# Performance work log

Measured on AMD Instinct MI355X. Metric: run time of the kernel, lower is better.

Reference implementation:

```python
import jax, jax.numpy as jnp
import numpy as np

N, DEG, D = 10000, 8, 128      # nodes, fixed out-degree, feature dim
E = N * DEG                    # graph edges = line-graph nodes
L = E * DEG                    # line-graph edges (fixed out-degree => exact)


def setup_inputs() -> dict:
    key = jax.random.key(0)
    kx, k1, k2 = jax.random.split(key, 3)
    rng = np.random.default_rng(0)

    # graph with fixed out-degree, no self-loops
    src = np.repeat(np.arange(N), DEG)                       # sorted by source
    dst = (src + 1 + rng.integers(0, N - 1, size=E)) % N
    edge_index = jnp.asarray(np.stack([src, dst]), dtype=jnp.int32)  # [2, E]

    # line graph: lg edge i -> j iff dst(i) == src(j)  (src(i)!=dst(i) holds for all i)
    # edges with source node v occupy indices v*DEG .. v*DEG+DEG-1
    lg_src = jnp.asarray(np.repeat(np.arange(E), DEG), dtype=jnp.int32)            # [L]
    lg_dst = jnp.asarray((dst[:, None] * DEG + np.arange(DEG)).reshape(-1),
                         dtype=jnp.int32)                                          # [L]

    x = jax.random.normal(kx, (N, D), jnp.float32)
    s = 1.0 / np.sqrt(D)
    ka, kb = jax.random.split(k1)
    W1 = jax.random.uniform(ka, (D, D), jnp.float32, -s, s)
    b1 = jnp.zeros((D,), jnp.float32)
    W2 = jax.random.uniform(kb, (D, D), jnp.float32, -s, s)
    b2 = jnp.zeros((D,), jnp.float32)
    return {"x": x, "edge_index": edge_index, "lg_src": lg_src, "lg_dst": lg_dst,
            "W1": W1, "b1": b1, "W2": W2, "b2": b2}


def reference(x, edge_index, lg_src, lg_dst, W1, b1, W2, b2):
    src, dst = edge_index[0], edge_index[1]
    # line-graph node features: mean of the two endpoint node features  [E, D]
    lgX = 0.5 * (x[src] + x[dst])
    # edge attr of lg edge (i->j) = feature of shared node = dst of source edge i  [L, D]
    edge_attr = x[dst[lg_src]]

    # 3 applications of the same GINEConv (eps=0, add aggregation)
    for _ in range(3):
        msg = jax.nn.relu(lgX[lg_src] + edge_attr)                      # [L, D]
        aggr = jax.ops.segment_sum(msg, lg_dst, num_segments=E)        # [E, D]
        h = lgX + aggr                                                  # (1+eps)*x_i + aggr, eps=0
        lgX = jax.nn.relu(h @ W1 + b1) @ W2 + b2

    # scatter_mean back to graph nodes over dst index, empty nodes -> 0 (matches pad)
    sums = jax.ops.segment_sum(lgX, dst, num_segments=N)               # [N, D]
    cnt = jax.ops.segment_sum(jnp.ones((E,), lgX.dtype), dst, num_segments=N)
    out = jax.nn.relu(sums / jnp.maximum(cnt, 1.0)[:, None])
    # dropout omitted (eval mode)
    return out
```

## Files before the change

kernel.cpp:

```cpp
#include <hip/hip_runtime.h>

#define NN 10000
#define EE 80000
#define DD 128
#define SLOTS 64

typedef short bf16x8 __attribute__((ext_vector_type(8)));
typedef float f32x4 __attribute__((ext_vector_type(4)));

__device__ __forceinline__ float b2f(uint u){ u <<= 16; return __builtin_bit_cast(float, u); }
__device__ __forceinline__ ushort f2b(float f){
  uint u = __builtin_bit_cast(uint, f);
  u += 0x7fffu + ((u >> 16) & 1u);
  return (ushort)(u >> 16);
}
__device__ __forceinline__ uint pack2(float a, float b){
  return (uint)f2b(a) | ((uint)f2b(b) << 16);
}

__global__ __launch_bounds__(256) void k_fill(const int* __restrict__ dst,
                                              int* __restrict__ cnt,
                                              int* __restrict__ inlist){
  int i = blockIdx.x * 256 + threadIdx.x;
  if (i < EE){
    int d = dst[i];
    int pos = atomicAdd(&cnt[d], 1);
    if (pos < SLOTS) inlist[d * SLOTS + pos] = i;
  }
}

__global__ __launch_bounds__(256) void k_wt(const float* __restrict__ W1, const float* __restrict__ W2,
                                            ushort* __restrict__ Wt1, ushort* __restrict__ Wt2){
  int idx = blockIdx.x * 256 + threadIdx.x;
  int which = idx >> 14;
  int r = idx & 16383;
  int k = r >> 7, n = r & 127;
  const float* W = which ? W2 : W1;
  ushort* Wt = which ? Wt2 : Wt1;
  Wt[n * DD + k] = f2b(W[r]);
}

__global__ __launch_bounds__(256) void k_init(const float* __restrict__ x, const int* __restrict__ dst,
                                              ushort* __restrict__ lgX){
  int tid = threadIdx.x;
  int i = blockIdx.x * 16 + (tid >> 4);
  int g = tid & 15;
  int s = i >> 3, d = dst[i];
  const float4* xs = (const float4*)(x + s * DD + g * 8);
  const float4* xd = (const float4*)(x + d * DD + g * 8);
  float4 s0 = xs[0], s1 = xs[1], d0 = xd[0], d1 = xd[1];
  uint4 o;
  o.x = pack2(0.5f * (s0.x + d0.x), 0.5f * (s0.y + d0.y));
  o.y = pack2(0.5f * (s0.z + d0.z), 0.5f * (s0.w + d0.w));
  o.z = pack2(0.5f * (s1.x + d1.x), 0.5f * (s1.y + d1.y));
  o.w = pack2(0.5f * (s1.z + d1.z), 0.5f * (s1.w + d1.w));
  *(uint4*)(lgX + i * DD + g * 8) = o;
}

__global__ __launch_bounds__(256) void k_aggr(const ushort* __restrict__ lgX, const float* __restrict__ x,
                                              const int* __restrict__ cnt, const int* __restrict__ inlist,
                                              float* __restrict__ A){
  int lane = threadIdx.x & 63;
  int v = blockIdx.x * 4 + (threadIdx.x >> 6);
  float2 xv = *(const float2*)(x + v * DD + lane * 2);
  int n = cnt[v]; if (n > SLOTS) n = SLOTS;
  float ax = 0.f, ay = 0.f;
  for (int t = 0; t < n; ++t){
    int e = inlist[v * SLOTS + t];
    uint u = *(const uint*)(lgX + e * DD + lane * 2);
    ax += fmaxf(b2f(u & 0xffffu) + xv.x, 0.f);
    ay += fmaxf(b2f(u >> 16)     + xv.y, 0.f);
  }
  float2 r; r.x = ax; r.y = ay;
  *(float2*)(A + v * DD + lane * 2) = r;
}

__global__ __launch_bounds__(256) void k_final(const ushort* __restrict__ lgX,
                                               const int* __restrict__ cnt, const int* __restrict__ inlist,
                                               float* __restrict__ out){
  int lane = threadIdx.x & 63;
  int v = blockIdx.x * 4 + (threadIdx.x >> 6);
  int n = cnt[v]; if (n > SLOTS) n = SLOTS;
  float ax = 0.f, ay = 0.f;
  for (int t = 0; t < n; ++t){
    int e = inlist[v * SLOTS + t];
    uint u = *(const uint*)(lgX + e * DD + lane * 2);
    ax += b2f(u & 0xffffu);
    ay += b2f(u >> 16);
  }
  float inv = 1.f / (float)(n > 0 ? n : 1);
  float2 r; r.x = fmaxf(ax * inv, 0.f); r.y = fmaxf(ay * inv, 0.f);
  *(float2*)(out + v * DD + lane * 2) = r;
}

__global__ __launch_bounds__(256, 2) void k_gemm(ushort* __restrict__ lgX, const float* __restrict__ A,
                                                 const ushort* __restrict__ Wt1, const ushort* __restrict__ Wt2,
                                                 const float* __restrict__ b1, const float* __restrict__ b2){
  __shared__ uint4 sm[4096];
  const int tid = threadIdx.x;
  const int lane = tid & 63;
  const int w = tid >> 6;
  const int rlo = lane & 15;
  const int khi = lane >> 4;
  const int row0 = blockIdx.x * 128;
  const bf16x8* smb = (const bf16x8*)sm;
  ushort* smh = (ushort*)sm;

  #pragma unroll
  for (int it = 0; it < 8; ++it){
    int gi = it * 256 + tid;
    int r = gi >> 4, g = gi & 15;
    sm[r * 16 + (g ^ (r & 7))] = *(const uint4*)(Wt1 + gi * 8);
  }
  #pragma unroll
  for (int p = 0; p < 8; ++p){
    int row = p * 16 + (tid >> 4);
    int g = tid & 15;
    int i = row0 + row;
    uint4 lx = *(const uint4*)(lgX + i * DD + g * 8);
    const float* Ap = A + (i >> 3) * DD + g * 8;
    float4 a0 = *(const float4*)Ap;
    float4 a1 = *(const float4*)(Ap + 4);
    uint uu[4] = {lx.x, lx.y, lx.z, lx.w};
    float av[8] = {a0.x, a0.y, a0.z, a0.w, a1.x, a1.y, a1.z, a1.w};
    float hv[8];
    #pragma unroll
    for (int j = 0; j < 4; ++j){
      hv[2*j]   = b2f(uu[j] & 0xffffu) + av[2*j];
      hv[2*j+1] = b2f(uu[j] >> 16)     + av[2*j+1];
    }
    uint4 o;
    o.x = pack2(hv[0], hv[1]); o.y = pack2(hv[2], hv[3]);
    o.z = pack2(hv[4], hv[5]); o.w = pack2(hv[6], hv[7]);
    sm[2048 + row * 16 + (g ^ (row & 7))] = o;
  }
  __syncthreads();

  f32x4 acc[2][8];
  #pragma unroll
  for (int m = 0; m < 2; ++m)
    #pragma unroll
    for (int nf = 0; nf < 8; ++nf) acc[m][nf] = (f32x4){0.f, 0.f, 0.f, 0.f};
  #pragma unroll
  for (int s = 0; s < 4; ++s){
    bf16x8 af[2];
    #pragma unroll
    for (int m = 0; m < 2; ++m){
      int row = 32 * w + 16 * m + rlo;
      int g = s * 4 + khi;
      af[m] = smb[2048 + row * 16 + (g ^ (row & 7))];
    }
    #pragma unroll
    for (int nf = 0; nf < 8; ++nf){
      int n = nf * 16 + rlo;
      int g = s * 4 + khi;
      bf16x8 bfr = smb[n * 16 + (g ^ (n & 7))];
      acc[0][nf] = __builtin_amdgcn_mfma_f32_16x16x32_bf16(af[0], bfr, acc[0][nf], 0, 0, 0);
      acc[1][nf] = __builtin_amdgcn_mfma_f32_16x16x32_bf16(af[1], bfr, acc[1][nf], 0, 0, 0);
    }
  }
  #pragma unroll
  for (int nf = 0; nf < 8; ++nf){
    float bb = b1[nf * 16 + rlo];
    #pragma unroll
    for (int m = 0; m < 2; ++m){
      #pragma unroll
      for (int q = 0; q < 4; ++q){
        float v = fmaxf(acc[m][nf][q] + bb, 0.f);
        int row = 32 * w + 16 * m + khi * 4 + q;
        int col = nf * 16 + rlo;
        smh[(2048 + row * 16 + ((col >> 3) ^ (row & 7))) * 8 + (col & 7)] = f2b(v);
      }
    }
  }
  __syncthreads();
  #pragma unroll
  for (int it = 0; it < 8; ++it){
    int gi = it * 256 + tid;
    int r = gi >> 4, g = gi & 15;
    sm[r * 16 + (g ^ (r & 7))] = *(const uint4*)(Wt2 + gi * 8);
  }
  __syncthreads();

  f32x4 acc2[2][8];
  #pragma unroll
  for (int m = 0; m < 2; ++m)
    #pragma unroll
    for (int nf = 0; nf < 8; ++nf) acc2[m][nf] = (f32x4){0.f, 0.f, 0.f, 0.f};
  #pragma unroll
  for (int s = 0; s < 4; ++s){
    bf16x8 af[2];
    #pragma unroll
    for (int m = 0; m < 2; ++m){
      int row = 32 * w + 16 * m + rlo;
      int g = s * 4 + khi;
      af[m] = smb[2048 + row * 16 + (g ^ (row & 7))];
    }
    #pragma unroll
    for (int nf = 0; nf < 8; ++nf){
      int n = nf * 16 + rlo;
      int g = s * 4 + khi;
      bf16x8 bfr = smb[n * 16 + (g ^ (n & 7))];
      acc2[0][nf] = __builtin_amdgcn_mfma_f32_16x16x32_bf16(af[0], bfr, acc2[0][nf], 0, 0, 0);
      acc2[1][nf] = __builtin_amdgcn_mfma_f32_16x16x32_bf16(af[1], bfr, acc2[1][nf], 0, 0, 0);
    }
  }
  #pragma unroll
  for (int nf = 0; nf < 8; ++nf){
    float bb = b2[nf * 16 + rlo];
    #pragma unroll
    for (int m = 0; m < 2; ++m){
      #pragma unroll
      for (int q = 0; q < 4; ++q){
        float v = acc2[m][nf][q] + bb;
        int row = 32 * w + 16 * m + khi * 4 + q;
        int col = nf * 16 + rlo;
        smh[(2048 + row * 16 + ((col >> 3) ^ (row & 7))) * 8 + (col & 7)] = f2b(v);
      }
    }
  }
  #pragma unroll
  for (int it = 0; it < 8; ++it){
    int u = it * 64 + lane;
    int row = 32 * w + (u >> 4);
    int g = u & 15;
    uint4 val = sm[2048 + row * 16 + (g ^ (row & 7))];
    *(uint4*)(lgX + (row0 + row) * DD + g * 8) = val;
  }
}

extern "C" void kernel_launch(void* const* d_in, const int* in_sizes, int n_in,
                              void* d_out, int out_size, void* d_ws, size_t ws_size,
                              hipStream_t stream){
  (void)in_sizes; (void)n_in; (void)out_size; (void)ws_size;
  const float* x  = (const float*)d_in[0];
  const int*   ei = (const int*)d_in[1];
  const int*   dst = ei + EE;
  const float* W1 = (const float*)d_in[4];
  const float* b1 = (const float*)d_in[5];
  const float* W2 = (const float*)d_in[6];
  const float* b2 = (const float*)d_in[7];
  float* out = (float*)d_out;

  char* ws = (char*)d_ws;
  ushort* lgX = (ushort*)ws;
  float*  A   = (float*)(ws + 20480000);
  ushort* Wt1 = (ushort*)(ws + 25600000);
  ushort* Wt2 = (ushort*)(ws + 25632768);
  int*    cnt = (int*)(ws + 25665536);
  int*    inl = (int*)(ws + 25705536);

  hipMemsetAsync(cnt, 0, NN * sizeof(int), stream);
  k_fill<<<(EE + 255) / 256, 256, 0, stream>>>(dst, cnt, inl);
  k_wt<<<128, 256, 0, stream>>>(W1, W2, Wt1, Wt2);
  k_init<<<EE / 16, 256, 0, stream>>>(x, dst, lgX);
  for (int it = 0; it < 3; ++it){
    k_aggr<<<NN / 4, 256, 0, stream>>>(lgX, x, cnt, inl, A);
    k_gemm<<<EE / 128, 256, 0, stream>>>(lgX, A, Wt1, Wt2, b1, b2);
  }
  k_final<<<NN / 4, 256, 0, stream>>>(lgX, cnt, inl, out);
}
```

Baseline: 212.5 us.

## Fuse setup kernels and restructure GEMM to keep H fragments in registers

```diff
diff --git a/kernel.cpp b/kernel.cpp
--- a/kernel.cpp
+++ b/kernel.cpp
@@ -18,43 +18,40 @@
   return (uint)f2b(a) | ((uint)f2b(b) << 16);
 }
 
-__global__ __launch_bounds__(256) void k_fill(const int* __restrict__ dst,
-                                              int* __restrict__ cnt,
-                                              int* __restrict__ inlist){
-  int i = blockIdx.x * 256 + threadIdx.x;
-  if (i < EE){
-    int d = dst[i];
-    int pos = atomicAdd(&cnt[d], 1);
-    if (pos < SLOTS) inlist[d * SLOTS + pos] = i;
-  }
-}
-
-__global__ __launch_bounds__(256) void k_wt(const float* __restrict__ W1, const float* __restrict__ W2,
-                                            ushort* __restrict__ Wt1, ushort* __restrict__ Wt2){
-  int idx = blockIdx.x * 256 + threadIdx.x;
-  int which = idx >> 14;
-  int r = idx & 16383;
-  int k = r >> 7, n = r & 127;
-  const float* W = which ? W2 : W1;
-  ushort* Wt = which ? Wt2 : Wt1;
-  Wt[n * DD + k] = f2b(W[r]);
-}
-
-__global__ __launch_bounds__(256) void k_init(const float* __restrict__ x, const int* __restrict__ dst,
-                                              ushort* __restrict__ lgX){
+__global__ __launch_bounds__(256) void k_pre(const float* __restrict__ x, const int* __restrict__ dst,
+                                             const float* __restrict__ W1, const float* __restrict__ W2,
+                                             ushort* __restrict__ lgX, ushort* __restrict__ Wt,
+                                             int* __restrict__ cnt, int* __restrict__ inlist){
+  int b = blockIdx.x;
   int tid = threadIdx.x;
-  int i = blockIdx.x * 16 + (tid >> 4);
-  int g = tid & 15;
-  int s = i >> 3, d = dst[i];
-  const float4* xs = (const float4*)(x + s * DD + g * 8);
-  const float4* xd = (const float4*)(x + d * DD + g * 8);
-  float4 s0 = xs[0], s1 = xs[1], d0 = xd[0], d1 = xd[1];
-  uint4 o;
-  o.x = pack2(0.5f * (s0.x + d0.x), 0.5f * (s0.y + d0.y));
-  o.y = pack2(0.5f * (s0.z + d0.z), 0.5f * (s0.w + d0.w));
-  o.z = pack2(0.5f * (s1.x + d1.x), 0.5f * (s1.y + d1.y));
-  o.w = pack2(0.5f * (s1.z + d1.z), 0.5f * (s1.w + d1.w));
-  *(uint4*)(lgX + i * DD + g * 8) = o;
+  if (b < 5000){
+    int i = b * 16 + (tid >> 4);
+    int g = tid & 15;
+    int s = i >> 3, d = dst[i];
+    const float4* xs = (const float4*)(x + s * DD + g * 8);
+    const float4* xd = (const float4*)(x + d * DD + g * 8);
+    float4 s0 = xs[0], s1 = xs[1], d0 = xd[0], d1 = xd[1];
+    uint4 o;
+    o.x = pack2(0.5f * (s0.x + d0.x), 0.5f * (s0.y + d0.y));
+    o.y = pack2(0.5f * (s0.z + d0.z), 0.5f * (s0.w + d0.w));
+    o.z = pack2(0.5f * (s1.x + d1.x), 0.5f * (s1.y + d1.y));
+    o.w = pack2(0.5f * (s1.z + d1.z), 0.5f * (s1.w + d1.w));
+    *(uint4*)(lgX + i * DD + g * 8) = o;
+  } else if (b < 5128){
+    int idx = (b - 5000) * 256 + tid;
+    int which = idx >> 14;
+    int r = idx & 16383;
+    int k = r >> 7, n = r & 127;
+    const float* W = which ? W2 : W1;
+    Wt[which * 16384 + n * DD + k] = f2b(W[r]);
+  } else {
+    int i = (b - 5128) * 256 + tid;
+    if (i < EE){
+      int d = dst[i];
+      int pos = atomicAdd(&cnt[d], 1);
+      if (pos < SLOTS) inlist[d * SLOTS + pos] = i;
+    }
+  }
 }
 
 __global__ __launch_bounds__(256) void k_aggr(const ushort* __restrict__ lgX, const float* __restrict__ x,
@@ -93,139 +90,137 @@
   *(float2*)(out + v * DD + lane * 2) = r;
 }
 
-__global__ __launch_bounds__(256, 2) void k_gemm(ushort* __restrict__ lgX, const float* __restrict__ A,
-                                                 const ushort* __restrict__ Wt1, const ushort* __restrict__ Wt2,
-                                                 const float* __restrict__ b1, const float* __restrict__ b2){
-  __shared__ uint4 sm[4096];
+__global__ __launch_bounds__(256) void k_gemm(ushort* __restrict__ lgX, const float* __restrict__ A,
+                                              const ushort* __restrict__ Wt,
+                                              const float* __restrict__ b1, const float* __restrict__ b2){
+  __shared__ uint4 smW[2048];
+  __shared__ uint4 smT[2048];
   const int tid = threadIdx.x;
   const int lane = tid & 63;
   const int w = tid >> 6;
   const int rlo = lane & 15;
   const int khi = lane >> 4;
   const int row0 = blockIdx.x * 128;
-  const bf16x8* smb = (const bf16x8*)sm;
-  ushort* smh = (ushort*)sm;
+  const bf16x8* smWb = (const bf16x8*)smW;
+  const bf16x8* smTb = (const bf16x8*)smT;
+  uint* smTu = (uint*)smT;
 
   #pragma unroll
   for (int it = 0; it < 8; ++it){
     int gi = it * 256 + tid;
     int r = gi >> 4, g = gi & 15;
-    sm[r * 16 + (g ^ (r & 7))] = *(const uint4*)(Wt1 + gi * 8);
-  }
-  #pragma unroll
-  for (int p = 0; p < 8; ++p){
-    int row = p * 16 + (tid >> 4);
-    int g = tid & 15;
-    int i = row0 + row;
-    uint4 lx = *(const uint4*)(lgX + i * DD + g * 8);
-    const float* Ap = A + (i >> 3) * DD + g * 8;
-    float4 a0 = *(const float4*)Ap;
-    float4 a1 = *(const float4*)(Ap + 4);
-    uint uu[4] = {lx.x, lx.y, lx.z, lx.w};
-    float av[8] = {a0.x, a0.y, a0.z, a0.w, a1.x, a1.y, a1.z, a1.w};
-    float hv[8];
-    #pragma unroll
-    for (int j = 0; j < 4; ++j){
-      hv[2*j]   = b2f(uu[j] & 0xffffu) + av[2*j];
-      hv[2*j+1] = b2f(uu[j] >> 16)     + av[2*j+1];
-    }
-    uint4 o;
-    o.x = pack2(hv[0], hv[1]); o.y = pack2(hv[2], hv[3]);
-    o.z = pack2(hv[4], hv[5]); o.w = pack2(hv[6], hv[7]);
-    sm[2048 + row * 16 + (g ^ (row & 7))] = o;
+    smW[r * 16 + (g ^ (r & 7))] = *(const uint4*)(Wt + gi * 8);
+  }
+
+  bf16x8 hfrag[2][4];
+  #pragma unroll
+  for (int mb = 0; mb < 2; ++mb){
+    int row = row0 + (2 * w + mb) * 16 + rlo;
+    const ushort* lp = lgX + row * DD;
+    const float*  ap = A + (row >> 3) * DD;
+    #pragma unroll
+    for (int s = 0; s < 4; ++s){
+      int k0 = s * 32 + khi * 8;
+      uint4 lx = *(const uint4*)(lp + k0);
+      float4 a0 = *(const float4*)(ap + k0);
+      float4 a1 = *(const float4*)(ap + k0 + 4);
+      uint uu[4] = {lx.x, lx.y, lx.z, lx.w};
+      float av[8] = {a0.x, a0.y, a0.z, a0.w, a1.x, a1.y, a1.z, a1.w};
+      uint4 o;
+      o.x = pack2(b2f(uu[0] & 0xffffu) + av[0], b2f(uu[0] >> 16) + av[1]);
+      o.y = pack2(b2f(uu[1] & 0xffffu) + av[2], b2f(uu[1] >> 16) + av[3]);
+      o.z = pack2(b2f(uu[2] & 0xffffu) + av[4], b2f(uu[2] >> 16) + av[5]);
+      o.w = pack2(b2f(uu[3] & 0xffffu) + av[6], b2f(uu[3] >> 16) + av[7]);
+      hfrag[mb][s] = __builtin_bit_cast(bf16x8, o);
+    }
   }
   __syncthreads();
 
-  f32x4 acc[2][8];
-  #pragma unroll
-  for (int m = 0; m < 2; ++m)
-    #pragma unroll
-    for (int nf = 0; nf < 8; ++nf) acc[m][nf] = (f32x4){0.f, 0.f, 0.f, 0.f};
+  f32x4 acc1[2][8];
+  #pragma unroll
+  for (int mb = 0; mb < 2; ++mb)
+    #pragma unroll
+    for (int nf = 0; nf < 8; ++nf) acc1[mb][nf] = (f32x4){0.f, 0.f, 0.f, 0.f};
   #pragma unroll
   for (int s = 0; s < 4; ++s){
-    bf16x8 af[2];
-    #pragma unroll
-    for (int m = 0; m < 2; ++m){
-      int row = 32 * w + 16 * m + rlo;
+    #pragma unroll
+    for (int nf = 0; nf < 8; ++nf){
+      int r = nf * 16 + rlo;
       int g = s * 4 + khi;
-      af[m] = smb[2048 + row * 16 + (g ^ (row & 7))];
-    }
-    #pragma unroll
-    for (int nf = 0; nf < 8; ++nf){
-      int n = nf * 16 + rlo;
+      bf16x8 wf = smWb[r * 16 + (g ^ (r & 7))];
+      acc1[0][nf] = __builtin_amdgcn_mfma_f32_16x16x32_bf16(wf, hfrag[0][s], acc1[0][nf], 0, 0, 0);
+      acc1[1][nf] = __builtin_amdgcn_mfma_f32_16x16x32_bf16(wf, hfrag[1][s], acc1[1][nf], 0, 0, 0);
+    }
+  }
+
+  #pragma unroll
+  for (int mb = 0; mb < 2; ++mb){
+    int row = (2 * w + mb) * 16 + rlo;
+    int rsw = row & 7;
+    #pragma unroll
+    for (int nf = 0; nf < 8; ++nf){
+      float4 bb = *(const float4*)(b1 + nf * 16 + khi * 4);
+      float t0 = fmaxf(acc1[mb][nf][0] + bb.x, 0.f);
+      float t1 = fmaxf(acc1[mb][nf][1] + bb.y, 0.f);
+      float t2 = fmaxf(acc1[mb][nf][2] + bb.z, 0.f);
+      float t3 = fmaxf(acc1[mb][nf][3] + bb.w, 0.f);
+      int u0 = nf * 8 + khi * 2;
+      int g0 = u0 >> 2;
+      int base = row * 64 + ((g0 ^ rsw) << 2) + (u0 & 3);
+      smTu[base]     = pack2(t0, t1);
+      smTu[base + 1] = pack2(t2, t3);
+    }
+  }
+
+  f32x4 acc2[2][8];
+  #pragma unroll
+  for (int mb = 0; mb < 2; ++mb)
+    #pragma unroll
+    for (int nf = 0; nf < 8; ++nf) acc2[mb][nf] = (f32x4){0.f, 0.f, 0.f, 0.f};
+  #pragma unroll
+  for (int s = 0; s < 4; ++s){
+    bf16x8 tf[2];
+    #pragma unroll
+    for (int mb = 0; mb < 2; ++mb){
+      int row = (2 * w + mb) * 16 + rlo;
       int g = s * 4 + khi;
-      bf16x8 bfr = smb[n * 16 + (g ^ (n & 7))];
-      acc[0][nf] = __builtin_amdgcn_mfma_f32_16x16x32_bf16(af[0], bfr, acc[0][nf], 0, 0, 0);
-      acc[1][nf] = __builtin_amdgcn_mfma_f32_16x16x32_bf16(af[1], bfr, acc[1][nf], 0, 0, 0);
-    }
-  }
-  #pragma unroll
-  for (int nf = 0; nf < 8; ++nf){
-    float bb = b1[nf * 16 + rlo];
-    #pragma unroll
-    for (int m = 0; m < 2; ++m){
-      #pragma unroll
-      for (int q = 0; q < 4; ++q){
-        float v = fmaxf(acc[m][nf][q] + bb, 0.f);
-        int row = 32 * w + 16 * m + khi * 4 + q;
-        int col = nf * 16 + rlo;
-        smh[(2048 + row * 16 + ((col >> 3) ^ (row & 7))) * 8 + (col & 7)] = f2b(v);
-      }
-    }
-  }
-  __syncthreads();
-  #pragma unroll
-  for (int it = 0; it < 8; ++it){
-    int gi = it * 256 + tid;
-    int r = gi >> 4, g = gi & 15;
-    sm[r * 16 + (g ^ (r & 7))] = *(const uint4*)(Wt2 + gi * 8);
-  }
-  __syncthreads();
-
-  f32x4 acc2[2][8];
-  #pragma unroll
-  for (int m = 0; m < 2; ++m)
-    #pragma unroll
-    for (int nf = 0; nf < 8; ++nf) acc2[m][nf] = (f32x4){0.f, 0.f, 0.f, 0.f};
-  #pragma unroll
-  for (int s = 0; s < 4; ++s){
-    bf16x8 af[2];
-    #pragma unroll
-    for (int m = 0; m < 2; ++m){
-      int row = 32 * w + 16 * m + rlo;
+      tf[mb] = smTb[row * 16 + (g ^ (row & 7))];
+    }
+    #pragma unroll
+    for (int nf = 0; nf < 8; ++nf){
+      bf16x8 wf = *(const bf16x8*)(Wt + 16384 + (nf * 16 + rlo) * DD + s * 32 + khi * 8);
+      acc2[0][nf] = __builtin_amdgcn_mfma_f32_16x16x32_bf16(wf, tf[0], acc2[0][nf], 0, 0, 0);
+      acc2[1][nf] = __builtin_amdgcn_mfma_f32_16x16x32_bf16(wf, tf[1], acc2[1][nf], 0, 0, 0);
+    }
+  }
+
+  #pragma unroll
+  for (int mb = 0; mb < 2; ++mb){
+    int row = (2 * w + mb) * 16 + rlo;
+    int rsw = row & 7;
+    #pragma unroll
+    for (int nf = 0; nf < 8; ++nf){
+      float4 bb = *(const float4*)(b2 + nf * 16 + khi * 4);
+      float t0 = acc2[mb][nf][0] + bb.x;
+      float t1 = acc2[mb][nf][1] + bb.y;
+      float t2 = acc2[mb][nf][2] + bb.z;
+      float t3 = acc2[mb][nf][3] + bb.w;
+      int u0 = nf * 8 + khi * 2;
+      int g0 = u0 >> 2;
+      int base = row * 64 + ((g0 ^ rsw) << 2) + (u0 & 3);
+      smTu[base]     = pack2(t0, t1);
+      smTu[base + 1] = pack2(t2, t3);
+    }
+  }
+  #pragma unroll
+  for (int mb = 0; mb < 2; ++mb){
+    int row = (2 * w + mb) * 16 + rlo;
+    #pragma unroll
+    for (int s = 0; s < 4; ++s){
       int g = s * 4 + khi;
-      af[m] = smb[2048 + row * 16 + (g ^ (row & 7))];
-    }
-    #pragma unroll
-    for (int nf = 0; nf < 8; ++nf){
-      int n = nf * 16 + rlo;
-      int g = s * 4 + khi;
-      bf16x8 bfr = smb[n * 16 + (g ^ (n & 7))];
-      acc2[0][nf] = __builtin_amdgcn_mfma_f32_16x16x32_bf16(af[0], bfr, acc2[0][nf], 0, 0, 0);
-      acc2[1][nf] = __builtin_amdgcn_mfma_f32_16x16x32_bf16(af[1], bfr, acc2[1][nf], 0, 0, 0);
-    }
-  }
-  #pragma unroll
-  for (int nf = 0; nf < 8; ++nf){
-    float bb = b2[nf * 16 + rlo];
-    #pragma unroll
-    for (int m = 0; m < 2; ++m){
-      #pragma unroll
-      for (int q = 0; q < 4; ++q){
-        float v = acc2[m][nf][q] + bb;
-        int row = 32 * w + 16 * m + khi * 4 + q;
-        int col = nf * 16 + rlo;
-        smh[(2048 + row * 16 + ((col >> 3) ^ (row & 7))) * 8 + (col & 7)] = f2b(v);
-      }
-    }
-  }
-  #pragma unroll
-  for (int it = 0; it < 8; ++it){
-    int u = it * 64 + lane;
-    int row = 32 * w + (u >> 4);
-    int g = u & 15;
-    uint4 val = sm[2048 + row * 16 + (g ^ (row & 7))];
-    *(uint4*)(lgX + (row0 + row) * DD + g * 8) = val;
+      uint4 val = smT[row * 16 + (g ^ (row & 7))];
+      *(uint4*)(lgX + (row0 + row) * DD + s * 32 + khi * 8) = val;
+    }
   }
 }
 
@@ -245,18 +240,15 @@
   char* ws = (char*)d_ws;
   ushort* lgX = (ushort*)ws;
   float*  A   = (float*)(ws + 20480000);
-  ushort* Wt1 = (ushort*)(ws + 25600000);
-  ushort* Wt2 = (ushort*)(ws + 25632768);
+  ushort* Wt  = (ushort*)(ws + 25600000);
   int*    cnt = (int*)(ws + 25665536);
   int*    inl = (int*)(ws + 25705536);
 
   hipMemsetAsync(cnt, 0, NN * sizeof(int), stream);
-  k_fill<<<(EE + 255) / 256, 256, 0, stream>>>(dst, cnt, inl);
-  k_wt<<<128, 256, 0, stream>>>(W1, W2, Wt1, Wt2);
-  k_init<<<EE / 16, 256, 0, stream>>>(x, dst, lgX);
+  k_pre<<<5441, 256, 0, stream>>>(x, dst, W1, W2, lgX, Wt, cnt, inl);
   for (int it = 0; it < 3; ++it){
     k_aggr<<<NN / 4, 256, 0, stream>>>(lgX, x, cnt, inl, A);
-    k_gemm<<<EE / 128, 256, 0, stream>>>(lgX, A, Wt1, Wt2, b1, b2);
+    k_gemm<<<EE / 128, 256, 0, stream>>>(lgX, A, Wt, b1, b2);
   }
   k_final<<<NN / 4, 256, 0, stream>>>(lgX, cnt, inl, out);
 }
```

New measurement: 229.2 us. 7.9% more time.
